# Kernel optimization log

Hardware: AMD Instinct MI355X
Metric: run time of the kernel (lower is better)

## Reference

```python
import jax, jax.numpy as jnp
import numpy as np

B, C, T = 32, 128, 16000
K = 2

def _conv1d(x, w, dil):
    # x: (N, C_in, T), w: (C_out, C_in, K)
    return jax.lax.conv_general_dilated(
        x, w, window_strides=(1,), padding='VALID',
        rhs_dilation=(dil,), dimension_numbers=('NCH', 'OIH', 'NCH'))

def setup_inputs() -> dict:
    key = jax.random.key(0)
    k1, k2, k3, k4 = jax.random.split(key, 4)
    s = 1.0 / np.sqrt(C * K)
    return {
        'x': jax.random.normal(k1, (B, C, T), dtype=jnp.float32),
        'w_filter': jax.random.normal(k2, (C, C, K), dtype=jnp.float32) * s,
        'w_gate': jax.random.normal(k3, (C, C, K), dtype=jnp.float32) * s,
        'w_skip': jax.random.normal(k4, (C, C, K), dtype=jnp.float32) * s,
        'dilation': 2,
    }

def reference(x, w_filter, w_gate, w_skip, dilation):
    residual = x
    # causal left pad by dilation -> dilated k=2 conv preserves length T
    xp = jnp.pad(x, ((0, 0), (0, 0), (dilation, 0)))
    o = jnp.tanh(_conv1d(xp, w_filter, dilation)) * jax.nn.sigmoid(_conv1d(xp, w_gate, dilation))
    # causal left pad by 1 -> k=2 dil=1 skip conv preserves length T
    op = jnp.pad(o, ((0, 0), (0, 0), (1, 0)))
    skip = _conv1d(op, w_skip, 1)
    out = skip + residual  # requires skip_channels == in_channels
    return (out, skip)
```

## Files before the change

### kernel.cpp

```cpp
#include <hip/hip_runtime.h>
#include <math.h>


#define CCH 128
#define TLEN 16000
#define NB 32
#define TT 63
#define XC 66
#define XTP 136
#define XSTRIDE 68
#define OSTRIDE 68

typedef __attribute__((ext_vector_type(8))) short bf16x8;
typedef __attribute__((ext_vector_type(4))) float f32x4;

__device__ __forceinline__ unsigned short f2bf(float f) {
    union { float f; unsigned u; } v; v.f = f;
    unsigned u = v.u + 0x7FFFu + ((v.u >> 16) & 1u);
    return (unsigned short)(u >> 16);
}
__device__ __forceinline__ float bf2f(unsigned short h) {
    union { float f; unsigned u; } v; v.u = ((unsigned)h) << 16;
    return v.f;
}

__global__ void prep_weights(const float* __restrict__ wf,
                             const float* __restrict__ wg,
                             const float* __restrict__ wsk,
                             unsigned short* __restrict__ wp)
{
    int idx = blockIdx.x * 256 + threadIdx.x;
    if (idx >= 3 * CCH * 256) return;
    int m   = idx >> 15;
    int rem = idx & 32767;
    int co  = rem >> 8;
    int kap = rem & 255;
    int tp = kap >> 7, ci = kap & 127;
    const float* w = (m == 0) ? wf : (m == 1) ? wg : wsk;
    float v = w[((size_t)co * CCH + ci) * 2 + tp];
    unsigned short h = f2bf(v);
    unsigned short lo = f2bf(v - bf2f(h));
    wp[(size_t)(2 * m)     * 32768 + rem] = h;
    wp[(size_t)(2 * m + 1) * 32768 + rem] = lo;
}

__global__ __launch_bounds__(256, 2)
void wavenet_mfma(const float* __restrict__ x,
                  const unsigned short* __restrict__ wp,
                  float* __restrict__ out,
                  float* __restrict__ skip)
{
    __shared__ unsigned short xTh[XC][XTP];
    __shared__ unsigned short xTl[XC][XTP];
    __shared__ unsigned short oTh[65][XTP];
    __shared__ unsigned short oTl[65][XTP];

    const int b   = blockIdx.y;
    const int ts  = blockIdx.x * TT;
    const int tid = threadIdx.x;

    const float* xb = x + (size_t)b * CCH * TLEN;
    for (int i = tid; i < CCH * XC; i += 256) {
        int ci = i / XC, c = i - ci * XC;
        int t = ts - 3 + c;
        float v = (t >= 0 && t < TLEN) ? xb[ci * TLEN + t] : 0.f;
        unsigned short h = f2bf(v);
        xTh[c][ci] = h;
        xTl[c][ci] = f2bf(v - bf2f(h));
    }
    if (tid < CCH) { oTh[64][tid] = 0; oTl[64][tid] = 0; }
    __syncthreads();

    const int l   = tid & 63;
    const int wv  = tid >> 6;
    const int li  = l & 15;
    const int lg  = l >> 4;
    const int coB = wv * 32;

    const unsigned short* Wfh = wp;
    const unsigned short* Wfl = wp + 32768;
    const unsigned short* Wgh = wp + 2 * 32768;
    const unsigned short* Wgl = wp + 3 * 32768;
    const unsigned short* Wsh = wp + 4 * 32768;
    const unsigned short* Wsl = wp + 5 * 32768;

    f32x4 accf[2][4], accg[2][4];
    #pragma unroll
    for (int rt = 0; rt < 2; ++rt)
        #pragma unroll
        for (int ct = 0; ct < 4; ++ct) {
            accf[rt][ct] = (f32x4){0.f, 0.f, 0.f, 0.f};
            accg[rt][ct] = (f32x4){0.f, 0.f, 0.f, 0.f};
        }

    for (int kc = 0; kc < 8; ++kc) {
        const int tp   = kc >> 2;
        const int ciq  = ((kc & 3) * 32) + lg * 8;
        const int kap0 = kc * 32 + lg * 8;
        bf16x8 afh[2], afl[2], agh[2], agl[2];
        #pragma unroll
        for (int rt = 0; rt < 2; ++rt) {
            const int off = (coB + rt * 16 + li) * 256 + kap0;
            afh[rt] = *(const bf16x8*)(Wfh + off);
            afl[rt] = *(const bf16x8*)(Wfl + off);
            agh[rt] = *(const bf16x8*)(Wgh + off);
            agl[rt] = *(const bf16x8*)(Wgl + off);
        }
        #pragma unroll
        for (int ct = 0; ct < 4; ++ct) {
            const int row = ct * 16 + li + 2 * tp;
            bf16x8 bh = *(const bf16x8*)&xTh[row][ciq];
            bf16x8 bl = *(const bf16x8*)&xTl[row][ciq];
            #pragma unroll
            for (int rt = 0; rt < 2; ++rt) {
                accf[rt][ct] = __builtin_amdgcn_mfma_f32_16x16x32_bf16(afh[rt], bh, accf[rt][ct], 0, 0, 0);
                accf[rt][ct] = __builtin_amdgcn_mfma_f32_16x16x32_bf16(afh[rt], bl, accf[rt][ct], 0, 0, 0);
                accf[rt][ct] = __builtin_amdgcn_mfma_f32_16x16x32_bf16(afl[rt], bh, accf[rt][ct], 0, 0, 0);
                accg[rt][ct] = __builtin_amdgcn_mfma_f32_16x16x32_bf16(agh[rt], bh, accg[rt][ct], 0, 0, 0);
                accg[rt][ct] = __builtin_amdgcn_mfma_f32_16x16x32_bf16(agh[rt], bl, accg[rt][ct], 0, 0, 0);
                accg[rt][ct] = __builtin_amdgcn_mfma_f32_16x16x32_bf16(agl[rt], bh, accg[rt][ct], 0, 0, 0);
            }
        }
    }

    #pragma unroll
    for (int rt = 0; rt < 2; ++rt)
        #pragma unroll
        for (int ct = 0; ct < 4; ++ct)
            #pragma unroll
            for (int r = 0; r < 4; ++r) {
                const float f = accf[rt][ct][r], g = accg[rt][ct][r];
                const float e2 = __expf(-2.f * f);
                const float th = (1.f - e2) / (1.f + e2);
                const float sg = 1.f / (1.f + __expf(-g));
                const float o = th * sg;
                const int co = coB + rt * 16 + lg * 4 + r;
                const int m  = ct * 16 + li;
                unsigned short h = f2bf(o);
                oTh[m][co] = h;
                oTl[m][co] = f2bf(o - bf2f(h));
            }
    __syncthreads();

    f32x4 accs[2][4];
    #pragma unroll
    for (int rt = 0; rt < 2; ++rt)
        #pragma unroll
        for (int ct = 0; ct < 4; ++ct)
            accs[rt][ct] = (f32x4){0.f, 0.f, 0.f, 0.f};

    for (int kc = 0; kc < 8; ++kc) {
        const int tp   = kc >> 2;
        const int ciq  = ((kc & 3) * 32) + lg * 8;
        const int kap0 = kc * 32 + lg * 8;
        bf16x8 ash[2], asl[2];
        #pragma unroll
        for (int rt = 0; rt < 2; ++rt) {
            const int off = (coB + rt * 16 + li) * 256 + kap0;
            ash[rt] = *(const bf16x8*)(Wsh + off);
            asl[rt] = *(const bf16x8*)(Wsl + off);
        }
        #pragma unroll
        for (int ct = 0; ct < 4; ++ct) {
            const int row = ct * 16 + li + tp;
            bf16x8 bh = *(const bf16x8*)&oTh[row][ciq];
            bf16x8 bl = *(const bf16x8*)&oTl[row][ciq];
            #pragma unroll
            for (int rt = 0; rt < 2; ++rt) {
                accs[rt][ct] = __builtin_amdgcn_mfma_f32_16x16x32_bf16(ash[rt], bh, accs[rt][ct], 0, 0, 0);
                accs[rt][ct] = __builtin_amdgcn_mfma_f32_16x16x32_bf16(ash[rt], bl, accs[rt][ct], 0, 0, 0);
                accs[rt][ct] = __builtin_amdgcn_mfma_f32_16x16x32_bf16(asl[rt], bh, accs[rt][ct], 0, 0, 0);
            }
        }
    }

    float* outb = out  + (size_t)b * CCH * TLEN;
    float* skb  = skip + (size_t)b * CCH * TLEN;
    #pragma unroll
    for (int rt = 0; rt < 2; ++rt)
        #pragma unroll
        for (int ct = 0; ct < 4; ++ct)
            #pragma unroll
            for (int r = 0; r < 4; ++r) {
                const int co = coB + rt * 16 + lg * 4 + r;
                const int jj = ct * 16 + li;
                const int t  = ts + jj;
                if (jj < TT && t < TLEN) {
                    const float s = accs[rt][ct][r];
                    const float xv = bf2f(xTh[jj + 3][co]) + bf2f(xTl[jj + 3][co]);
                    outb[(size_t)co * TLEN + t] = s + xv;
                    skb [(size_t)co * TLEN + t] = s;
                }
            }
}

__global__ __launch_bounds__(256, 2)
void wavenet_fused_f32(const float* __restrict__ x,
                       const float* __restrict__ wf,
                       const float* __restrict__ wg,
                       const float* __restrict__ wsk,
                       float* __restrict__ out,
                       float* __restrict__ skip)
{
    __shared__ float xs[CCH][XSTRIDE];
    __shared__ float os[CCH][OSTRIDE];

    const int b  = blockIdx.y;
    const int ts = blockIdx.x * TT;
    const int tid = threadIdx.x;

    const float* xb = x + (size_t)b * CCH * TLEN;
    for (int i = tid; i < CCH * XC; i += 256) {
        const int ch = i / XC, col = i % XC;
        const int t = ts - 3 + col;
        float v = 0.f;
        if (t >= 0 && t < TLEN) v = xb[ch * TLEN + t];
        xs[ch][col] = v;
    }
    __syncthreads();

    const int tg  = tid & 15;
    const int cg  = tid >> 4;
    const int tl  = tg * 4;
    const int co0 = cg * 8;

    float ff[8][4], gg[8][4];
    #pragma unroll
    for (int c = 0; c < 8; ++c)
        #pragma unroll
        for (int j = 0; j < 4; ++j) { ff[c][j] = 0.f; gg[c][j] = 0.f; }

    for (int ci = 0; ci < CCH; ci += 2) {
        const float4 a0 = *(const float4*)&xs[ci][tl];
        const float4 a1 = *(const float4*)&xs[ci][tl + 4];
        const float4 b0 = *(const float4*)&xs[ci + 1][tl];
        const float4 b1 = *(const float4*)&xs[ci + 1][tl + 4];
        const float t0a[4] = {a0.x, a0.y, a0.z, a0.w};
        const float t1a[4] = {a0.z, a0.w, a1.x, a1.y};
        const float t0b[4] = {b0.x, b0.y, b0.z, b0.w};
        const float t1b[4] = {b0.z, b0.w, b1.x, b1.y};
        #pragma unroll
        for (int c = 0; c < 8; ++c) {
            const float4 w4f = *(const float4*)&wf[((size_t)(co0 + c) * CCH + ci) * 2];
            const float4 w4g = *(const float4*)&wg[((size_t)(co0 + c) * CCH + ci) * 2];
            #pragma unroll
            for (int j = 0; j < 4; ++j) {
                ff[c][j] = fmaf(w4f.x, t0a[j], ff[c][j]);
                ff[c][j] = fmaf(w4f.y, t1a[j], ff[c][j]);
                ff[c][j] = fmaf(w4f.z, t0b[j], ff[c][j]);
                ff[c][j] = fmaf(w4f.w, t1b[j], ff[c][j]);
                gg[c][j] = fmaf(w4g.x, t0a[j], gg[c][j]);
                gg[c][j] = fmaf(w4g.y, t1a[j], gg[c][j]);
                gg[c][j] = fmaf(w4g.z, t0b[j], gg[c][j]);
                gg[c][j] = fmaf(w4g.w, t1b[j], gg[c][j]);
            }
        }
    }

    #pragma unroll
    for (int c = 0; c < 8; ++c) {
        float4 ov;
        float* po = (float*)&ov;
        #pragma unroll
        for (int j = 0; j < 4; ++j) {
            const float f = ff[c][j], g = gg[c][j];
            const float e2 = __expf(-2.f * f);
            const float th = (1.f - e2) / (1.f + e2);
            const float sg = 1.f / (1.f + __expf(-g));
            po[j] = th * sg;
        }
        *(float4*)&os[co0 + c][tl] = ov;
    }
    __syncthreads();

    float sk[8][4];
    #pragma unroll
    for (int c = 0; c < 8; ++c)
        #pragma unroll
        for (int j = 0; j < 4; ++j) sk[c][j] = 0.f;

    for (int ci = 0; ci < CCH; ci += 2) {
        const float4 a0 = *(const float4*)&os[ci][tl];
        const float4 a1 = *(const float4*)&os[ci][tl + 4];
        const float4 b0 = *(const float4*)&os[ci + 1][tl];
        const float4 b1 = *(const float4*)&os[ci + 1][tl + 4];
        const float t0a[4] = {a0.x, a0.y, a0.z, a0.w};
        const float t1a[4] = {a0.y, a0.z, a0.w, a1.x};
        const float t0b[4] = {b0.x, b0.y, b0.z, b0.w};
        const float t1b[4] = {b0.y, b0.z, b0.w, b1.x};
        #pragma unroll
        for (int c = 0; c < 8; ++c) {
            const float4 w4s = *(const float4*)&wsk[((size_t)(co0 + c) * CCH + ci) * 2];
            #pragma unroll
            for (int j = 0; j < 4; ++j) {
                sk[c][j] = fmaf(w4s.x, t0a[j], sk[c][j]);
                sk[c][j] = fmaf(w4s.y, t1a[j], sk[c][j]);
                sk[c][j] = fmaf(w4s.z, t0b[j], sk[c][j]);
                sk[c][j] = fmaf(w4s.w, t1b[j], sk[c][j]);
            }
        }
    }

    float* outb = out  + (size_t)b * CCH * TLEN;
    float* skb  = skip + (size_t)b * CCH * TLEN;
    #pragma unroll
    for (int c = 0; c < 8; ++c) {
        #pragma unroll
        for (int j = 0; j < 4; ++j) {
            const int jj = tl + j;
            const int t  = ts + jj;
            if (jj < TT && t < TLEN) {
                const float s = sk[c][j];
                outb[(size_t)(co0 + c) * TLEN + t] = s + xs[co0 + c][jj + 3];
                skb [(size_t)(co0 + c) * TLEN + t] = s;
            }
        }
    }
}

extern "C" void kernel_launch(void* const* d_in, const int* in_sizes, int n_in,
                              void* d_out, int out_size, void* d_ws, size_t ws_size,
                              hipStream_t stream) {
    const float* x   = (const float*)d_in[0];
    const float* wf  = (const float*)d_in[1];
    const float* wg  = (const float*)d_in[2];
    const float* wsk = (const float*)d_in[3];

    float* out  = (float*)d_out;
    float* skip = out + (size_t)NB * CCH * TLEN;

    dim3 grid((TLEN + TT - 1) / TT, NB);

    const size_t ws_needed = (size_t)6 * 32768 * sizeof(unsigned short);
    if (ws_size < ws_needed) {
        wavenet_fused_f32<<<grid, 256, 0, stream>>>(x, wf, wg, wsk, out, skip);
        return;
    }

    unsigned short* wp = (unsigned short*)d_ws;
    prep_weights<<<dim3(384), 256, 0, stream>>>(wf, wg, wsk, wp);
    wavenet_mfma<<<grid, 256, 0, stream>>>(x, wp, out, skip);
}
```

Baseline: 1.304 ms.

## Alias x and o tiles in shared memory to raise occupancy

Merges the input and intermediate shared-memory tiles into one aliased buffer, roughly halving LDS per block, and raises the launch bound to four blocks per CU. An extra barrier separates the last read of the x tile from the o writes, and the residual is re-read from global memory instead of LDS. The tanh·sigmoid expression is folded into a single division. The higher launch bound limits registers, which may cause spills given the large accumulator arrays, and the residual re-read adds global traffic.

New measurement: 1.205 ms. -7.6%, faster.

```diff
diff --git a/kernel.cpp b/kernel.cpp
--- a/kernel.cpp
+++ b/kernel.cpp
@@ -44,31 +44,28 @@
     wp[(size_t)(2 * m + 1) * 32768 + rem] = lo;
 }
 
-__global__ __launch_bounds__(256, 2)
+__global__ __launch_bounds__(256, 4)
 void wavenet_mfma(const float* __restrict__ x,
                   const unsigned short* __restrict__ wp,
                   float* __restrict__ out,
                   float* __restrict__ skip)
 {
-    __shared__ unsigned short xTh[XC][XTP];
-    __shared__ unsigned short xTl[XC][XTP];
-    __shared__ unsigned short oTh[65][XTP];
-    __shared__ unsigned short oTl[65][XTP];
+    __shared__ unsigned short sh[2][XC][XTP];
 
     const int b   = blockIdx.y;
     const int ts  = blockIdx.x * TT;
     const int tid = threadIdx.x;
 
     const float* xb = x + (size_t)b * CCH * TLEN;
-    for (int i = tid; i < CCH * XC; i += 256) {
+    for (int k = 0; k < 33; ++k) {
+        int i = tid + k * 256;
         int ci = i / XC, c = i - ci * XC;
         int t = ts - 3 + c;
         float v = (t >= 0 && t < TLEN) ? xb[ci * TLEN + t] : 0.f;
         unsigned short h = f2bf(v);
-        xTh[c][ci] = h;
-        xTl[c][ci] = f2bf(v - bf2f(h));
-    }
-    if (tid < CCH) { oTh[64][tid] = 0; oTl[64][tid] = 0; }
+        sh[0][c][ci] = h;
+        sh[1][c][ci] = f2bf(v - bf2f(h));
+    }
     __syncthreads();
 
     const int l   = tid & 63;
@@ -109,8 +106,8 @@
         #pragma unroll
         for (int ct = 0; ct < 4; ++ct) {
             const int row = ct * 16 + li + 2 * tp;
-            bf16x8 bh = *(const bf16x8*)&xTh[row][ciq];
-            bf16x8 bl = *(const bf16x8*)&xTl[row][ciq];
+            bf16x8 bh = *(const bf16x8*)&sh[0][row][ciq];
+            bf16x8 bl = *(const bf16x8*)&sh[1][row][ciq];
             #pragma unroll
             for (int rt = 0; rt < 2; ++rt) {
                 accf[rt][ct] = __builtin_amdgcn_mfma_f32_16x16x32_bf16(afh[rt], bh, accf[rt][ct], 0, 0, 0);
@@ -123,6 +120,9 @@
         }
     }
 
+    __syncthreads();
+
+    if (tid < CCH) { sh[0][64][tid] = 0; sh[1][64][tid] = 0; }
     #pragma unroll
     for (int rt = 0; rt < 2; ++rt)
         #pragma unroll
@@ -131,14 +131,13 @@
             for (int r = 0; r < 4; ++r) {
                 const float f = accf[rt][ct][r], g = accg[rt][ct][r];
                 const float e2 = __expf(-2.f * f);
-                const float th = (1.f - e2) / (1.f + e2);
-                const float sg = 1.f / (1.f + __expf(-g));
-                const float o = th * sg;
+                const float eg = __expf(-g);
+                const float o = (1.f - e2) / ((1.f + e2) * (1.f + eg));
                 const int co = coB + rt * 16 + lg * 4 + r;
                 const int m  = ct * 16 + li;
                 unsigned short h = f2bf(o);
-                oTh[m][co] = h;
-                oTl[m][co] = f2bf(o - bf2f(h));
+                sh[0][m][co] = h;
+                sh[1][m][co] = f2bf(o - bf2f(h));
             }
     __syncthreads();
 
@@ -163,8 +162,8 @@
         #pragma unroll
         for (int ct = 0; ct < 4; ++ct) {
             const int row = ct * 16 + li + tp;
-            bf16x8 bh = *(const bf16x8*)&oTh[row][ciq];
-            bf16x8 bl = *(const bf16x8*)&oTl[row][ciq];
+            bf16x8 bh = *(const bf16x8*)&sh[0][row][ciq];
+            bf16x8 bl = *(const bf16x8*)&sh[1][row][ciq];
             #pragma unroll
             for (int rt = 0; rt < 2; ++rt) {
                 accs[rt][ct] = __builtin_amdgcn_mfma_f32_16x16x32_bf16(ash[rt], bh, accs[rt][ct], 0, 0, 0);
@@ -187,7 +186,7 @@
                 const int t  = ts + jj;
                 if (jj < TT && t < TLEN) {
                     const float s = accs[rt][ct][r];
-                    const float xv = bf2f(xTh[jj + 3][co]) + bf2f(xTl[jj + 3][co]);
+                    const float xv = xb[(size_t)co * TLEN + t];
                     outb[(size_t)co * TLEN + t] = s + xv;
                     skb [(size_t)co * TLEN + t] = s;
                 }
```
